# Kernel tuning notes

Hardware: AMD Instinct MI355X
Metric: run time of the kernel (lower is better)

The kernel has to match this reference:

```python
import jax, jax.numpy as jnp
import numpy as np

N_NODES = 50000
DIM = 64
HEADS = 4
N_EDGES = 800000
NEG_SLOPE = 0.2  # PyG GATConv default


def setup_inputs() -> dict:
    key = jax.random.key(0)
    ks = jax.random.split(key, 8)
    H, C = HEADS, DIM
    embedding = jax.random.normal(ks[0], (N_NODES, DIM), dtype=jnp.float32)
    graph = jax.random.randint(ks[1], (2, N_EDGES), 0, N_NODES, dtype=jnp.int64)
    s = 1.0 / np.sqrt(DIM)
    # GATConv params: shared source/target linear (PyG uses one lin when in_channels is int)
    W = jax.random.normal(ks[2], (DIM, H * C), dtype=jnp.float32) * s
    att_src = jax.random.normal(ks[3], (H, C), dtype=jnp.float32) * s
    att_dst = jax.random.normal(ks[4], (H, C), dtype=jnp.float32) * s
    bias = jnp.zeros((H * C,), dtype=jnp.float32)
    # dense: Linear(dim*heads -> dim)
    dense_w = jax.random.normal(ks[5], (H * C, DIM), dtype=jnp.float32) / np.sqrt(H * C)
    dense_b = jnp.zeros((DIM,), dtype=jnp.float32)
    return {"embedding": embedding, "graph": graph, "W": W, "att_src": att_src,
            "att_dst": att_dst, "bias": bias, "dense_w": dense_w, "dense_b": dense_b}


def reference(embedding, graph, W, att_src, att_dst, bias, dense_w, dense_b):
    N, D = embedding.shape
    H, C = att_src.shape
    # linear projection, per-head view: [N, H, C]
    x = (embedding @ W).reshape(N, H, C)
    # add self loops (PyG default add_self_loops=True)
    ar = jnp.arange(N, dtype=graph.dtype)
    src = jnp.concatenate([graph[0], ar])  # [E+N]
    dst = jnp.concatenate([graph[1], ar])
    # per-node attention logits, gathered per edge
    a_src = jnp.einsum('nhc,hc->nh', x, att_src)  # [N, H]
    a_dst = jnp.einsum('nhc,hc->nh', x, att_dst)
    alpha = jax.nn.leaky_relu(a_src[src] + a_dst[dst], NEG_SLOPE)  # [E, H]
    # segment softmax over destination nodes
    amax = jax.ops.segment_max(alpha, dst, num_segments=N)  # [N, H]
    amax = jnp.where(jnp.isfinite(amax), amax, 0.0)
    ex = jnp.exp(alpha - amax[dst])
    denom = jax.ops.segment_sum(ex, dst, num_segments=N)
    coef = ex / (denom[dst] + 1e-16)  # [E, H]
    # weighted scatter-aggregate of source features
    msg = x[src] * coef[:, :, None]  # [E, H, C]
    agg = jax.ops.segment_sum(msg, dst, num_segments=N)  # [N, H, C]
    gat_out = agg.reshape(N, H * C) + bias  # concat heads + bias
    return gat_out @ dense_w + dense_b  # [N, D]
```

## Files before the change

kernel.cpp:

```cpp
#include <hip/hip_runtime.h>
#include <hip/hip_fp16.h>
#include <cfloat>
#include <cmath>

#define DIM 64
#define HEADS 4
#define NEG 0.2f
#define CAP 64

__device__ __forceinline__ float lrelu(float a) { return a > 0.0f ? a : NEG * a; }

__device__ __forceinline__ unsigned pack_half2(float a, float b) {
    return (unsigned)__half_as_ushort(__float2half(a)) |
           ((unsigned)__half_as_ushort(__float2half(b)) << 16);
}

__global__ __launch_bounds__(256) void prep_kernel(
        const float* __restrict__ W, const float* __restrict__ dw,
        const float* __restrict__ att_s, const float* __restrict__ att_d,
        const float* __restrict__ bias, const float* __restrict__ db,
        const float* __restrict__ emb,
        float* __restrict__ M, float* __restrict__ bvec,
        float* __restrict__ a_src, float* __restrict__ a_dst,
        float* __restrict__ pself, int* __restrict__ cnt, int N) {
    const int b = blockIdx.x, t = threadIdx.x;
    if (b < 64) {
        __shared__ float s_W[256];
        s_W[t] = W[b * 256 + t];
        __syncthreads();
        const int h = t >> 6, j = t & 63;
        float s = 0.f;
        for (int c = 0; c < 64; c++)
            s = fmaf(s_W[h * 64 + c], dw[(h * 64 + c) * 64 + j], s);
        M[b * 256 + t] = s;
    } else if (b == 64) {
        __shared__ float s_p[256];
        const int j = t & 63, kq = t >> 6;
        float p = 0.f;
        for (int k = kq * 64; k < kq * 64 + 64; k++)
            p = fmaf(bias[k], dw[k * 64 + j], p);
        s_p[t] = p;
        __syncthreads();
        if (t < 64)
            bvec[t] = s_p[t] + s_p[64 + t] + s_p[128 + t] + s_p[192 + t] + db[t];
    } else {
        __shared__ float s_e[64 * 68];
        __shared__ float s_vs[256], s_vd[256];
        const int n0 = (b - 65) * 64;
        {
            const int d = t >> 2, h = t & 3;
            const float4* w4 = (const float4*)(W + d * 256 + h * 64);
            const float4* s4 = (const float4*)(att_s + h * 64);
            const float4* d4 = (const float4*)(att_d + h * 64);
            float vs = 0.f, vd = 0.f;
#pragma unroll
            for (int k = 0; k < 16; k++) {
                float4 w = w4[k], as = s4[k], ad = d4[k];
                vs = fmaf(w.x, as.x, fmaf(w.y, as.y, fmaf(w.z, as.z, fmaf(w.w, as.w, vs))));
                vd = fmaf(w.x, ad.x, fmaf(w.y, ad.y, fmaf(w.z, ad.z, fmaf(w.w, ad.w, vd))));
            }
            s_vs[h * 64 + d] = vs;
            s_vd[h * 64 + d] = vd;
        }
#pragma unroll
        for (int r = 0; r < 4; r++) {
            int idx = (r * 256 + t) * 4;
            int i = idx >> 6, d = idx & 63;
            int row = min(n0 + i, N - 1);
            *(float4*)(s_e + i * 68 + d) = *(const float4*)(emb + (size_t)row * 64 + d);
        }
        __syncthreads();
        const int node = t >> 2, h = t & 3;
        const float* er = s_e + node * 68;
        float as = 0.f, ad = 0.f;
#pragma unroll
        for (int g = 0; g < 16; g++) {
            float4 ev = *(const float4*)(er + 4 * g);
            float4 vs = *(const float4*)(s_vs + h * 64 + 4 * g);
            float4 vd = *(const float4*)(s_vd + h * 64 + 4 * g);
            as = fmaf(ev.x, vs.x, fmaf(ev.y, vs.y, fmaf(ev.z, vs.z, fmaf(ev.w, vs.w, as))));
            ad = fmaf(ev.x, vd.x, fmaf(ev.y, vd.y, fmaf(ev.z, vd.z, fmaf(ev.w, vd.w, ad))));
        }
        const int n = n0 + node;
        if (n < N) {
            a_src[(size_t)n * 4 + h] = as;
            a_dst[(size_t)n * 4 + h] = ad;
            pself[(size_t)n * 4 + h] = __expf(lrelu(as + ad));
        }
        if (t < 64 && n0 + t < N) cnt[n0 + t] = 0;
    }
}

__global__ __launch_bounds__(256) void mid_kernel(
        const int* __restrict__ gsrc, const int* __restrict__ gdst,
        const float* __restrict__ a_src, const float* __restrict__ a_dst,
        int* __restrict__ cnt, uint4* __restrict__ rec,
        const float* __restrict__ emb, const float* __restrict__ M,
        unsigned* __restrict__ y32, int E, int N, int FB) {
    __shared__ float s_e[64 * 68];
    const int t = threadIdx.x;

    if ((int)blockIdx.x < FB) {
        const int e0 = (blockIdx.x * 256 + t) * 4;
        if (e0 >= E) return;
        int4 s4, d4;
        if (e0 + 3 < E) {
            s4 = *(const int4*)(gsrc + e0);
            d4 = *(const int4*)(gdst + e0);
        } else {
            int* sp = (int*)&s4; int* dp = (int*)&d4;
            for (int k = 0; k < 4; k++) {
                int e = min(e0 + k, E - 1);
                sp[k] = gsrc[e]; dp[k] = gdst[e];
            }
        }
        const int nk = min(4, E - e0);
#pragma unroll
        for (int k = 0; k < 4; k++) {
            if (k >= nk) break;
            const int s = ((const int*)&s4)[k];
            const int d = ((const int*)&d4)[k];
            float4 as = *(const float4*)(a_src + (size_t)s * 4);
            float4 ad = *(const float4*)(a_dst + (size_t)d * 4);
            uint4 r;
            r.x = (unsigned)s;
            r.y = pack_half2(__expf(lrelu(as.x + ad.x)), __expf(lrelu(as.y + ad.y)));
            r.z = pack_half2(__expf(lrelu(as.z + ad.z)), __expf(lrelu(as.w + ad.w)));
            r.w = 0u;
            int pos = atomicAdd(&cnt[d], 1);
            if (pos < CAP) rec[(size_t)d * CAP + pos] = r;
        }
        return;
    }

    const int l = t & 63;
    const int wq = __builtin_amdgcn_readfirstlane(t >> 6);
    const int n0 = (blockIdx.x - FB) * 64;

#pragma unroll
    for (int r = 0; r < 4; r++) {
        int idx = (r * 256 + t) * 4;
        int i = idx >> 6, d = idx & 63;
        int row = min(n0 + i, N - 1);
        *(float4*)(s_e + i * 68 + d) = *(const float4*)(emb + (size_t)row * 64 + d);
    }
    __syncthreads();

    float4 acc[16];
#pragma unroll
    for (int i = 0; i < 16; i++) acc[i] = make_float4(0.f, 0.f, 0.f, 0.f);

    const float* eb = s_e + wq * 16 * 68;

    for (int g = 0; g < 16; g++) {
        const int d0 = g * 4;
        float4 wv0 = *(const float4*)(M + (d0 + 0) * 256 + 4 * l);
        float4 wv1 = *(const float4*)(M + (d0 + 1) * 256 + 4 * l);
        float4 wv2 = *(const float4*)(M + (d0 + 2) * 256 + 4 * l);
        float4 wv3 = *(const float4*)(M + (d0 + 3) * 256 + 4 * l);
#pragma unroll
        for (int i = 0; i < 16; i++) {
            float4 ev = *(const float4*)(eb + i * 68 + d0);
            acc[i].x = fmaf(ev.x, wv0.x, acc[i].x);
            acc[i].y = fmaf(ev.x, wv0.y, acc[i].y);
            acc[i].z = fmaf(ev.x, wv0.z, acc[i].z);
            acc[i].w = fmaf(ev.x, wv0.w, acc[i].w);
            acc[i].x = fmaf(ev.y, wv1.x, acc[i].x);
            acc[i].y = fmaf(ev.y, wv1.y, acc[i].y);
            acc[i].z = fmaf(ev.y, wv1.z, acc[i].z);
            acc[i].w = fmaf(ev.y, wv1.w, acc[i].w);
            acc[i].x = fmaf(ev.z, wv2.x, acc[i].x);
            acc[i].y = fmaf(ev.z, wv2.y, acc[i].y);
            acc[i].z = fmaf(ev.z, wv2.z, acc[i].z);
            acc[i].w = fmaf(ev.z, wv2.w, acc[i].w);
            acc[i].x = fmaf(ev.w, wv3.x, acc[i].x);
            acc[i].y = fmaf(ev.w, wv3.y, acc[i].y);
            acc[i].z = fmaf(ev.w, wv3.z, acc[i].z);
            acc[i].w = fmaf(ev.w, wv3.w, acc[i].w);
        }
    }

#pragma unroll
    for (int i = 0; i < 16; i++) {
        int n = n0 + wq * 16 + i;
        if (n < N) {
            uint2 u;
            u.x = pack_half2(acc[i].x, acc[i].y);
            u.y = pack_half2(acc[i].z, acc[i].w);
            *(uint2*)(y32 + (size_t)n * 128 + 2 * l) = u;
        }
    }
}

__global__ __launch_bounds__(256) void aggregate_kernel(
        const int* __restrict__ cnt, const uint4* __restrict__ rec,
        const float* __restrict__ pself,
        const unsigned* __restrict__ y32, const float* __restrict__ bvec,
        float* __restrict__ out, int N) {
    const int t = threadIdx.x;
    const int l = t & 63;
    const int dd = blockIdx.x * 4 + (t >> 6);
    if (dd >= N) return;
    const int d = __builtin_amdgcn_readfirstlane(dd);
    const int hl = l >> 4;
    const int deg = min(__builtin_amdgcn_readfirstlane(cnt[d]), CAP);
    const uint4* rb = rec + (size_t)d * CAP;
    const unsigned* yl = y32 + 2 * l;

    float p = pself[(size_t)d * 4 + hl];
    uint2 v = *(const uint2*)(yl + (size_t)d * 128);
    float2 f0 = __half22float2(*(const __half2*)&v.x);
    float2 f1 = __half22float2(*(const __half2*)&v.y);
    float den = p;
    float ax = p * f0.x, ay = p * f0.y, az = p * f1.x, aw = p * f1.y;

#pragma unroll 4
    for (int i = 0; i < deg; i++) {
        const uint4 r = rb[i];
        const unsigned ph = (hl & 2) ? r.z : r.y;
        const unsigned sh = (hl & 1) ? (ph >> 16) : (ph & 0xffffu);
        const float pe = __half2float(__ushort_as_half((unsigned short)sh));
        const uint2 vv = *(const uint2*)(yl + (size_t)r.x * 128);
        float2 g0 = __half22float2(*(const __half2*)&vv.x);
        float2 g1 = __half22float2(*(const __half2*)&vv.y);
        den += pe;
        ax = fmaf(pe, g0.x, ax);
        ay = fmaf(pe, g0.y, ay);
        az = fmaf(pe, g1.x, az);
        aw = fmaf(pe, g1.y, aw);
    }

    const float inv = 1.0f / (den + 1e-16f);
    float rx = ax * inv, ry = ay * inv, rz = az * inv, rw = aw * inv;
    rx += __shfl_xor(rx, 16, 64); ry += __shfl_xor(ry, 16, 64);
    rz += __shfl_xor(rz, 16, 64); rw += __shfl_xor(rw, 16, 64);
    rx += __shfl_xor(rx, 32, 64); ry += __shfl_xor(ry, 32, 64);
    rz += __shfl_xor(rz, 32, 64); rw += __shfl_xor(rw, 32, 64);
    if (l < 16) {
        float4 bv = *(const float4*)(bvec + 4 * l);
        float4 r;
        r.x = rx + bv.x; r.y = ry + bv.y; r.z = rz + bv.z; r.w = rw + bv.w;
        *(float4*)(out + (size_t)dd * 64 + 4 * l) = r;
    }
}

extern "C" void kernel_launch(void* const* d_in, const int* in_sizes, int n_in,
                              void* d_out, int out_size, void* d_ws, size_t ws_size,
                              hipStream_t stream) {
    const float* emb   = (const float*)d_in[0];
    const int*   graph = (const int*)d_in[1];
    const float* W     = (const float*)d_in[2];
    const float* att_s = (const float*)d_in[3];
    const float* att_d = (const float*)d_in[4];
    const float* bias  = (const float*)d_in[5];
    const float* dw    = (const float*)d_in[6];
    const float* db    = (const float*)d_in[7];
    float* out = (float*)d_out;

    const int N = in_sizes[0] / DIM;
    const int E = in_sizes[1] / 2;
    const int* gsrc = graph;
    const int* gdst = graph + E;

    unsigned* y32  = (unsigned*)d_ws;
    uint4* rec     = (uint4*)(y32 + (size_t)N * 128);
    float* a_src   = (float*)(rec + (size_t)N * CAP);
    float* a_dst   = a_src + (size_t)N * 4;
    float* pself   = a_dst + (size_t)N * 4;
    float* M       = pself + (size_t)N * 4;
    float* bvec    = M + 64 * 256;
    int*   cnt     = (int*)(bvec + 64);

    const int quads = (E + 3) / 4;
    const int FB = (quads + 255) / 256;
    const int PB = (N + 63) / 64;

    hipLaunchKernelGGL(prep_kernel, dim3(65 + PB), dim3(256), 0, stream,
                       W, dw, att_s, att_d, bias, db, emb,
                       M, bvec, a_src, a_dst, pself, cnt, N);
    hipLaunchKernelGGL(mid_kernel, dim3(FB + PB), dim3(256), 0, stream,
                       gsrc, gdst, a_src, a_dst, cnt, rec,
                       emb, M, y32, E, N, FB);
    hipLaunchKernelGGL(aggregate_kernel, dim3((N + 3) / 4), dim3(256), 0, stream,
                       cnt, rec, pself, y32, bvec, out, N);
}
```

Measured before the change: 217.6 us.

## Store only source indices in edge buckets; compute attention weights in aggregate

The scatter phase now writes a 4-byte source index per edge instead of a 16-byte record with precomputed fp16 exp-weights, and no longer gathers a_src/a_dst per edge. The aggregate kernel reads bucket indices eight at a time as vectors, broadcasts them via readfirstlane, gathers a_src for each source and computes the exp-leaky-relu weight in fp32. This cuts bucket write and read traffic and removes the fp16 rounding of weights. In exchange the aggregate kernel does an extra dependent gather and an exp per edge per lane, and the vector loads may read past deg within the CAP-sized bucket.

```diff
diff --git a/kernel.cpp b/kernel.cpp
--- a/kernel.cpp
+++ b/kernel.cpp
@@ -93,8 +93,7 @@
 
 __global__ __launch_bounds__(256) void mid_kernel(
         const int* __restrict__ gsrc, const int* __restrict__ gdst,
-        const float* __restrict__ a_src, const float* __restrict__ a_dst,
-        int* __restrict__ cnt, uint4* __restrict__ rec,
+        int* __restrict__ cnt, unsigned* __restrict__ rec,
         const float* __restrict__ emb, const float* __restrict__ M,
         unsigned* __restrict__ y32, int E, int N, int FB) {
     __shared__ float s_e[64 * 68];
@@ -120,15 +119,8 @@
             if (k >= nk) break;
             const int s = ((const int*)&s4)[k];
             const int d = ((const int*)&d4)[k];
-            float4 as = *(const float4*)(a_src + (size_t)s * 4);
-            float4 ad = *(const float4*)(a_dst + (size_t)d * 4);
-            uint4 r;
-            r.x = (unsigned)s;
-            r.y = pack_half2(__expf(lrelu(as.x + ad.x)), __expf(lrelu(as.y + ad.y)));
-            r.z = pack_half2(__expf(lrelu(as.z + ad.z)), __expf(lrelu(as.w + ad.w)));
-            r.w = 0u;
-            int pos = atomicAdd(&cnt[d], 1);
-            if (pos < CAP) rec[(size_t)d * CAP + pos] = r;
+            const int pos = atomicAdd(&cnt[d], 1);
+            if (pos < CAP) rec[(size_t)d * CAP + pos] = (unsigned)s;
         }
         return;
     }
@@ -193,7 +185,8 @@
 }
 
 __global__ __launch_bounds__(256) void aggregate_kernel(
-        const int* __restrict__ cnt, const uint4* __restrict__ rec,
+        const int* __restrict__ cnt, const unsigned* __restrict__ rec,
+        const float* __restrict__ a_src, const float* __restrict__ a_dst,
         const float* __restrict__ pself,
         const unsigned* __restrict__ y32, const float* __restrict__ bvec,
         float* __restrict__ out, int N) {
@@ -204,8 +197,9 @@
     const int d = __builtin_amdgcn_readfirstlane(dd);
     const int hl = l >> 4;
     const int deg = min(__builtin_amdgcn_readfirstlane(cnt[d]), CAP);
-    const uint4* rb = rec + (size_t)d * CAP;
+    const unsigned* rb = rec + (size_t)d * CAP;
     const unsigned* yl = y32 + 2 * l;
+    const float adh = a_dst[(size_t)d * 4 + hl];
 
     float p = pself[(size_t)d * 4 + hl];
     uint2 v = *(const uint2*)(yl + (size_t)d * 128);
@@ -214,20 +208,33 @@
     float den = p;
     float ax = p * f0.x, ay = p * f0.y, az = p * f1.x, aw = p * f1.y;
 
-#pragma unroll 4
-    for (int i = 0; i < deg; i++) {
-        const uint4 r = rb[i];
-        const unsigned ph = (hl & 2) ? r.z : r.y;
-        const unsigned sh = (hl & 1) ? (ph >> 16) : (ph & 0xffffu);
-        const float pe = __half2float(__ushort_as_half((unsigned short)sh));
-        const uint2 vv = *(const uint2*)(yl + (size_t)r.x * 128);
-        float2 g0 = __half22float2(*(const __half2*)&vv.x);
-        float2 g1 = __half22float2(*(const __half2*)&vv.y);
-        den += pe;
-        ax = fmaf(pe, g0.x, ax);
-        ay = fmaf(pe, g0.y, ay);
-        az = fmaf(pe, g1.x, az);
-        aw = fmaf(pe, g1.y, aw);
+    for (int c0 = 0; c0 < deg; c0 += 8) {
+        const int cn = min(8, deg - c0);
+        uint4 r0 = *(const uint4*)(rb + c0);
+        uint4 r1 = (cn > 4) ? *(const uint4*)(rb + c0 + 4) : r0;
+        int ss[8];
+#pragma unroll
+        for (int k = 0; k < 4; k++) {
+            ss[k]     = __builtin_amdgcn_readfirstlane((int)((const unsigned*)&r0)[k]);
+            ss[k + 4] = __builtin_amdgcn_readfirstlane((int)((const unsigned*)&r1)[k]);
+        }
+#pragma unroll
+        for (int k = 0; k < 8; k++) {
+            if (k >= cn) break;
+            const int s = ss[k];
+            const float4 as4 = *(const float4*)(a_src + (size_t)s * 4);
+            const float ash = (hl & 2) ? ((hl & 1) ? as4.w : as4.z)
+                                       : ((hl & 1) ? as4.y : as4.x);
+            const float pe = __expf(lrelu(ash + adh));
+            const uint2 vv = *(const uint2*)(yl + (size_t)s * 128);
+            float2 g0 = __half22float2(*(const __half2*)&vv.x);
+            float2 g1 = __half22float2(*(const __half2*)&vv.y);
+            den += pe;
+            ax = fmaf(pe, g0.x, ax);
+            ay = fmaf(pe, g0.y, ay);
+            az = fmaf(pe, g1.x, az);
+            aw = fmaf(pe, g1.y, aw);
+        }
     }
 
     const float inv = 1.0f / (den + 1e-16f);
@@ -263,7 +270,7 @@
     const int* gdst = graph + E;
 
     unsigned* y32  = (unsigned*)d_ws;
-    uint4* rec     = (uint4*)(y32 + (size_t)N * 128);
+    unsigned* rec  = y32 + (size_t)N * 128;
     float* a_src   = (float*)(rec + (size_t)N * CAP);
     float* a_dst   = a_src + (size_t)N * 4;
     float* pself   = a_dst + (size_t)N * 4;
@@ -279,8 +286,8 @@
                        W, dw, att_s, att_d, bias, db, emb,
                        M, bvec, a_src, a_dst, pself, cnt, N);
     hipLaunchKernelGGL(mid_kernel, dim3(FB + PB), dim3(256), 0, stream,
-                       gsrc, gdst, a_src, a_dst, cnt, rec,
+                       gsrc, gdst, cnt, rec,
                        emb, M, y32, E, N, FB);
     hipLaunchKernelGGL(aggregate_kernel, dim3((N + 3) / 4), dim3(256), 0, stream,
-                       cnt, rec, pself, y32, bvec, out, N);
-}
+                       cnt, rec, a_src, a_dst, pself, y32, bvec, out, N);
+}
```

Measured after the change: 257.2 us. 1.18x slower.
